# Kernel optimization log

Measured on AMD Instinct MI355X. Metric: run time of the kernel, lower is better.

The kernel has to match this reference:

```python
import jax, jax.numpy as jnp
import numpy as np
from jax import lax

B, C, H, W = 4, 24, 128, 128
R = 7
NUM_CLASSES = 6
MAX_STEPS = 8


def _conv(x, w, b, pad):
    y = lax.conv_general_dilated(x, w, (1, 1), [(pad, pad), (pad, pad)],
                                 dimension_numbers=("NCHW", "OIHW", "NCHW"))
    return y + b[None, :, None, None]


def setup_inputs() -> dict:
    key = jax.random.key(0)
    ks = jax.random.split(key, 16)
    s = 0.05
    inp = {
        "depth_latent": jax.random.normal(ks[0], (B, C, H, W), jnp.float32),
        "texture_features": jax.random.normal(ks[1], (B, 3, H, W), jnp.float32),
        "class_labels": jax.random.randint(ks[2], (B,), 0, NUM_CLASSES),
        # texture_encoder
        "w_te1": jax.random.normal(ks[3], (64, 3, 3, 3), jnp.float32) * s,
        "b_te1": jnp.zeros((64,), jnp.float32),
        "w_te2": jax.random.normal(ks[4], (128, 64, 3, 3), jnp.float32) * s,
        "b_te2": jnp.zeros((128,), jnp.float32),
        # class embedding [num_classes, 128]
        "emb": jax.random.normal(ks[5], (NUM_CLASSES, 128), jnp.float32) * s,
        # fusion_layer: Conv2d(256,256,3) -> Conv2d(256, C*R*R, 1)
        "w_f1": jax.random.normal(ks[6], (256, 256, 3, 3), jnp.float32) * s,
        "b_f1": jnp.zeros((256,), jnp.float32),
        "w_f2": jax.random.normal(ks[7], (C * R * R, 256, 1, 1), jnp.float32) * s,
        "b_f2": jnp.zeros((C * R * R,), jnp.float32),
        # class_gate: Conv2d(128,64,3) -> Conv2d(64,num_classes,1)
        "w_g1": jax.random.normal(ks[8], (64, 128, 3, 3), jnp.float32) * s,
        "b_g1": jnp.zeros((64,), jnp.float32),
        "w_g2": jax.random.normal(ks[9], (NUM_CLASSES, 64, 1, 1), jnp.float32) * s,
        "b_g2": jnp.zeros((NUM_CLASSES,), jnp.float32),
        "class_intensity": jnp.ones((1, NUM_CLASSES, 1, 1), jnp.float32),
    }
    return inp


def _forward(depth_latent, texture_features, class_labels,
             w_te1, b_te1, w_te2, b_te2, emb,
             w_f1, b_f1, w_f2, b_f2,
             w_g1, b_g1, w_g2, b_g2, class_intensity):
    pad = R // 2
    # texture encoder
    tex = jax.nn.relu(_conv(texture_features, w_te1, b_te1, 1))
    tex = jax.nn.relu(_conv(tex, w_te2, b_te2, 1))  # [B,128,H,W]

    # 1-D integer class label path
    class_cond = jax.nn.one_hot(class_labels, NUM_CLASSES, dtype=jnp.float32)[:, :, None, None]  # [B,K,1,1]
    class_emb = emb[class_labels][:, :, None, None]  # [B,128,1,1]

    gate = jax.nn.sigmoid(_conv(jax.nn.relu(_conv(tex, w_g1, b_g1, 1)), w_g2, b_g2, 0))
    class_gate = gate * class_cond  # [B,K,H,W]

    fused = jnp.concatenate([tex, jnp.broadcast_to(class_emb, (tex.shape[0], 128, H, W))], axis=1)
    weights = _conv(jax.nn.relu(_conv(fused, w_f1, b_f1, 1)), w_f2, b_f2, 0)
    weights = weights.reshape(-1, C, R * R, H, W)

    intensity_map = (class_gate * class_intensity).sum(axis=1, keepdims=True)  # [B,1,H,W]
    weights = weights * intensity_map[:, :, None]  # [B,C,R*R,H,W]
    weights = jax.nn.softmax(weights, axis=2)

    def diffusion_step(lat):
        p = jnp.pad(lat, ((0, 0), (0, 0), (pad, pad), (pad, pad)), mode="edge")
        # unfold order: kernel row-major (i*R + j)
        windows = jnp.stack([p[:, :, i:i + H, j:j + W]
                             for i in range(R) for j in range(R)], axis=2)
        return (windows * weights).sum(axis=2)

    enhanced = lax.fori_loop(0, MAX_STEPS, lambda _, lat: diffusion_step(lat), depth_latent)

    condition_map = intensity_map * class_gate.sum(axis=1, keepdims=True)
    return enhanced, class_gate, condition_map


def reference(depth_latent, texture_features, class_labels,
              w_te1, b_te1, w_te2, b_te2, emb,
              w_f1, b_f1, w_f2, b_f2,
              w_g1, b_g1, w_g2, b_g2, class_intensity):
    return _forward(depth_latent, texture_features, class_labels,
                    w_te1, b_te1, w_te2, b_te2, emb,
                    w_f1, b_f1, w_f2, b_f2,
                    w_g1, b_g1, w_g2, b_g2, class_intensity)
```

## Files before the change

kernel.cpp:

```cpp
#include <hip/hip_runtime.h>
#include <hip/hip_bf16.h>
#include <stdint.h>

#define DINL __device__ __forceinline__

DINL float bf2f(__hip_bfloat16 v) { return __bfloat162float(v); }
DINL __hip_bfloat16 f2bf(float v) { return __float2bfloat16(v); }
DINL float bflo(unsigned int u) { return __uint_as_float(u << 16); }
DINL float bfhi(unsigned int u) { return __uint_as_float(u & 0xffff0000u); }

DINL float loadf(float v) { return v; }
DINL float loadf(__hip_bfloat16 v) { return __bfloat162float(v); }

typedef __attribute__((ext_vector_type(8))) short bf16x8;
typedef __attribute__((ext_vector_type(4))) float f32x4;

#define O_WTE1 0
#define O_WG2  1792
#define O_SS   2304
#define O_INT  11520
#define BO_W2B   308224u
#define BO_TE2B 1094656u
#define BO_WG1B 1242112u
#define BO_WF1B 1389568u
#define BO_TEX  4194304u
#define BO_F1   20971520u
#define BO_PING 54525952u
#define BO_PONG 60817408u
#define BO_W    67108864u
#define BO_T1   BO_W
#define BO_G1   (BO_W + 16777216u)

__global__ __launch_bounds__(256) void prep_kernel(
    const float* __restrict__ w_te1, const float* __restrict__ w_te2,
    const float* __restrict__ w_g1,  const float* __restrict__ w_f1,
    const float* __restrict__ w_f2,  const float* __restrict__ w_g2,
    const float* __restrict__ emb,   const int* __restrict__ labels,
    float* __restrict__ wsf)
{
  const int gid = blockIdx.x * 256 + threadIdx.x;
  const int stride = gridDim.x * 256;
  const int A0 = 1728, A1 = A0 + 393216, A2 = A1 + 73728, A3 = A2 + 73728,
            A4 = A3 + 294912, A5 = A4 + 384;
  __hip_bfloat16* w2b  = (__hip_bfloat16*)((char*)wsf + BO_W2B);
  __hip_bfloat16* te2b = (__hip_bfloat16*)((char*)wsf + BO_TE2B);
  __hip_bfloat16* g1b  = (__hip_bfloat16*)((char*)wsf + BO_WG1B);
  __hip_bfloat16* f1b  = (__hip_bfloat16*)((char*)wsf + BO_WF1B);
  for (int i = gid; i < A5; i += stride) {
    if (i < A0) {
      int s = i; int o = s / 27; int r = s - o * 27; int ic = r / 9; int t = r - ic * 9;
      wsf[O_WTE1 + (((o >> 5) * 3 + ic) * 9 + t) * 32 + (o & 31)] = w_te1[s];
    } else if (i < A1) {
      int s = i - A0;
      int j = s & 7; int lane = (s >> 3) & 63; int ks = (s >> 9) & 7;
      int wv = (s >> 12) & 3; int c = s >> 14;
      int tap = wv * 16 + (lane & 15);
      int k = ks * 32 + (lane >> 4) * 8 + j;
      float v = (tap < 49) ? w_f2[(c * 49 + tap) * 256 + k] : 0.f;
      w2b[s] = f2bf(v);
    } else if (i < A2) {
      int s = i - A1;
      int k = s & 31; int n = (s >> 5) & 63; int u = s >> 11;
      int t = u % 9; int v = u / 9; int kc = v & 1; int ocg = v >> 1;
      te2b[s] = f2bf(w_te2[((ocg * 64 + n) * 64 + kc * 32 + k) * 9 + t]);
    } else if (i < A3) {
      int s = i - A2;
      int k = s & 31; int n = (s >> 5) & 63; int u = s >> 11;
      int t = u % 9; int kc = u / 9;
      g1b[s] = f2bf(w_g1[(n * 128 + kc * 32 + k) * 9 + t]);
    } else if (i < A4) {
      int s = i - A3;
      int k = s & 31; int n = (s >> 5) & 63; int u = s >> 11;
      int t = u % 9; int v = u / 9; int kc = v & 3; int ocg = v >> 2;
      f1b[s] = f2bf(w_f1[((ocg * 64 + n) * 256 + kc * 32 + k) * 9 + t]);
    } else {
      int s = i - A4;
      wsf[O_WG2 + s] = w_g2[s];
    }
  }
  if (gid < 1024) {
    int b = gid >> 8, o = gid & 255;
    int lab = labels[b];
    float St[9];
#pragma unroll
    for (int t = 0; t < 9; ++t) St[t] = 0.f;
    for (int i = 0; i < 128; ++i) {
      float e = emb[lab * 128 + i];
#pragma unroll
      for (int t = 0; t < 9; ++t)
        St[t] += w_f1[(o * 256 + 128 + i) * 9 + t] * e;
    }
#pragma unroll
    for (int ch = 0; ch < 3; ++ch)
#pragma unroll
      for (int cw = 0; cw < 3; ++cw) {
        float sum = 0.f;
#pragma unroll
        for (int t = 0; t < 9; ++t) {
          int kh = t / 3, kw = t - kh * 3;
          bool ok = !(ch == 0 && kh == 0) && !(ch == 2 && kh == 2) &&
                    !(cw == 0 && kw == 0) && !(cw == 2 && kw == 2);
          if (ok) sum += St[t];
        }
        wsf[O_SS + gid * 9 + ch * 3 + cw] = sum;
      }
  }
}

template<typename TIn, int ICH, bool PIXMAJOR>
__global__ __launch_bounds__(256, 2) void conv3x3_kernel(
    const TIn* __restrict__ in, const float* __restrict__ wf,
    const float* __restrict__ bias,
    __hip_bfloat16* __restrict__ out, const int och_total)
{
  constexpr int CH = (ICH < 16) ? ICH : 16;
  constexpr int NCHUNK = ICH / CH;
  __shared__ TIn sIn[CH][18][20];
  const int tid = threadIdx.x;
  const int b = blockIdx.z;
  const int ob = blockIdx.y;
  const int och0 = ob * 32;
  const int tileY = blockIdx.x >> 3, tileX = blockIdx.x & 7;
  const int ty = tid >> 4, tx = tid & 15;
  const int h = tileY * 16 + ty, w = tileX * 16 + tx;
  const int h0 = tileY * 16 - 1, w0 = tileX * 16 - 1;

  float acc[32];
#pragma unroll
  for (int o = 0; o < 32; ++o) acc[o] = bias[och0 + o];

  for (int cc = 0; cc < NCHUNK; ++cc) {
    if (cc) __syncthreads();
    for (int e = tid; e < CH * 324; e += 256) {
      int ic = e / 324, r = e - ic * 324;
      int y = r / 18, x = r - y * 18;
      int gh = h0 + y, gw = w0 + x;
      TIn v = TIn(0.f);
      if ((unsigned)gh < 128u && (unsigned)gw < 128u)
        v = in[((b * ICH + cc * CH + ic) << 14) + (gh << 7) + gw];
      sIn[ic][y][x] = v;
    }
    __syncthreads();
#pragma unroll 1
    for (int ic = 0; ic < CH; ++ic) {
      const float* wrow = wf + (ob * ICH + cc * CH + ic) * 288;
#pragma unroll
      for (int t = 0; t < 9; ++t) {
        const int kh = t / 3, kw = t - kh * 3;
        const float v = loadf(sIn[ic][ty + kh][tx + kw]);
#pragma unroll
        for (int o = 0; o < 32; ++o)
          acc[o] = fmaf(wrow[t * 32 + o], v, acc[o]);
      }
    }
  }

  const int pix = (h << 7) + w;
  if constexpr (!PIXMAJOR) {
#pragma unroll
    for (int o = 0; o < 32; ++o)
      out[((b * och_total + och0 + o) << 14) + pix] = f2bf(fmaxf(acc[o], 0.f));
  } else {
    union { uint4 u4[4]; __hip_bfloat16 hh[32]; } pk;
#pragma unroll
    for (int o = 0; o < 32; ++o) pk.hh[o] = f2bf(fmaxf(acc[o], 0.f));
    uint4* dst = reinterpret_cast<uint4*>(out + ((size_t)(b << 14) + pix) * och_total + och0);
#pragma unroll
    for (int i = 0; i < 4; ++i) dst[i] = pk.u4[i];
  }
}

template<int ICH, bool ADD_SS>
__global__ __launch_bounds__(256, 2) void conv3x3_mfma_kernel(
    const __hip_bfloat16* __restrict__ in, const __hip_bfloat16* __restrict__ wb,
    const float* __restrict__ bias, const float* __restrict__ SS,
    __hip_bfloat16* __restrict__ out, const int och_total)
{
  constexpr int NKC = ICH / 32;
  __shared__ __hip_bfloat16 sH[324][40];
  __shared__ __hip_bfloat16 sW[9][64][40];
  const int tid = threadIdx.x, b = blockIdx.z, ocg = blockIdx.y;
  const int tileY = blockIdx.x >> 3, tileX = blockIdx.x & 7;
  const int h0 = tileY * 16 - 1, w0 = tileX * 16 - 1;
  const int wave = tid >> 6, lane = tid & 63, m16 = lane & 15, quad = lane >> 4;

  f32x4 acc[4][4];
#pragma unroll
  for (int i = 0; i < 4; ++i)
#pragma unroll
    for (int j = 0; j < 4; ++j) acc[i][j] = f32x4{0.f, 0.f, 0.f, 0.f};

  for (int kc = 0; kc < NKC; ++kc) {
    if (kc) __syncthreads();
    for (int e = tid; e < 1296; e += 256) {
      int pos = e >> 2, q = e & 3;
      int y = pos / 18, x = pos - y * 18;
      int gh = h0 + y, gw = w0 + x;
      uint4 v = uint4{0u, 0u, 0u, 0u};
      if ((unsigned)gh < 128u && (unsigned)gw < 128u)
        v = *(const uint4*)(in + ((size_t)((b << 14) + (gh << 7) + gw)) * ICH + kc * 32 + q * 8);
      *(uint4*)&sH[pos][q * 8] = v;
    }
    const uint4* wsrc = (const uint4*)(wb + ((size_t)(ocg * NKC + kc)) * 9 * 64 * 32);
    for (int e = tid; e < 2304; e += 256) {
      int q = e & 3, n = (e >> 2) & 63, t = e >> 8;
      *(uint4*)&sW[t][n][q * 8] = wsrc[e];
    }
    __syncthreads();
#pragma unroll
    for (int t = 0; t < 9; ++t) {
      const int dy = t / 3, dx = t - dy * 3;
      bf16x8 bfr[4];
#pragma unroll
      for (int nt = 0; nt < 4; ++nt)
        bfr[nt] = *(const bf16x8*)&sW[t][nt * 16 + m16][quad * 8];
#pragma unroll
      for (int mi = 0; mi < 4; ++mi) {
        const int py = wave * 4 + mi;
        const bf16x8 afr = *(const bf16x8*)&sH[(py + dy) * 18 + dx + m16][quad * 8];
#pragma unroll
        for (int nt = 0; nt < 4; ++nt)
          acc[mi][nt] = __builtin_amdgcn_mfma_f32_16x16x32_bf16(afr, bfr[nt], acc[mi][nt], 0, 0, 0);
      }
    }
  }

  float bv[4];
#pragma unroll
  for (int nt = 0; nt < 4; ++nt) bv[nt] = bias[ocg * 64 + nt * 16 + m16];
#pragma unroll
  for (int mi = 0; mi < 4; ++mi) {
    const int py = wave * 4 + mi;
    const int h = tileY * 16 + py;
    const int chc = (h == 0) ? 0 : ((h == 127) ? 2 : 1);
#pragma unroll
    for (int nt = 0; nt < 4; ++nt) {
      float sr0 = 0.f, sr1 = 0.f, sr2 = 0.f;
      if constexpr (ADD_SS) {
        const float* sp = SS + ((size_t)(b << 8) + (ocg * 64 + nt * 16 + m16)) * 9;
        sr0 = sp[chc * 3 + 0]; sr1 = sp[chc * 3 + 1]; sr2 = sp[chc * 3 + 2];
      }
      const int och = ocg * 64 + nt * 16 + m16;
#pragma unroll
      for (int r = 0; r < 4; ++r) {
        const int px = quad * 4 + r;
        const int w = tileX * 16 + px;
        float v = acc[mi][nt][r] + bv[nt];
        if constexpr (ADD_SS)
          v += (w == 0) ? sr0 : ((w == 127) ? sr2 : sr1);
        v = fmaxf(v, 0.f);
        out[((size_t)((b << 14) + (h << 7) + w)) * och_total + och] = f2bf(v);
      }
    }
  }
}

__global__ __launch_bounds__(256) void gate2_kernel(
    const __hip_bfloat16* __restrict__ g1, const float* __restrict__ wg2,
    const float* __restrict__ b_g2, const int* __restrict__ labels,
    const float* __restrict__ ci,
    float* __restrict__ out_cg, float* __restrict__ out_cond,
    float* __restrict__ inten)
{
  const int b = blockIdx.y;
  const int pix = blockIdx.x * 256 + threadIdx.x;
  float acc[6];
#pragma unroll
  for (int k = 0; k < 6; ++k) acc[k] = b_g2[k];
  const uint4* gp = (const uint4*)(g1 + ((size_t)((b << 14) + pix)) * 64);
#pragma unroll
  for (int i4 = 0; i4 < 8; ++i4) {
    const uint4 q = gp[i4];
    const float v0 = bflo(q.x), v1 = bfhi(q.x), v2 = bflo(q.y), v3 = bfhi(q.y);
    const float v4 = bflo(q.z), v5 = bfhi(q.z), v6 = bflo(q.w), v7 = bfhi(q.w);
#pragma unroll
    for (int k = 0; k < 6; ++k) {
      const float* wr = wg2 + k * 64 + i4 * 8;
      acc[k] = fmaf(wr[0], v0, acc[k]); acc[k] = fmaf(wr[1], v1, acc[k]);
      acc[k] = fmaf(wr[2], v2, acc[k]); acc[k] = fmaf(wr[3], v3, acc[k]);
      acc[k] = fmaf(wr[4], v4, acc[k]); acc[k] = fmaf(wr[5], v5, acc[k]);
      acc[k] = fmaf(wr[6], v6, acc[k]); acc[k] = fmaf(wr[7], v7, acc[k]);
    }
  }
  const int lab = labels[b];
  float gate[6], gl = 0.f;
#pragma unroll
  for (int k = 0; k < 6; ++k) {
    gate[k] = 1.f / (1.f + __expf(-acc[k]));
    gl = (k == lab) ? gate[k] : gl;
  }
  const float civ = ci[lab];
  const float it = gl * civ;
#pragma unroll
  for (int k = 0; k < 6; ++k)
    out_cg[((b * 6 + k) << 14) + pix] = (k == lab) ? gate[k] : 0.f;
  inten[(b << 14) + pix] = it;
  out_cond[(b << 14) + pix] = it * gl;
}

__global__ __launch_bounds__(256, 2) void gemm_softmax_kernel(
    const __hip_bfloat16* __restrict__ f1, const __hip_bfloat16* __restrict__ w2b,
    const float* __restrict__ b_f2, const float* __restrict__ inten,
    __hip_bfloat16* __restrict__ wout)
{
  __shared__ float sL[49 * 65];
  __shared__ float sR1[256];
  __shared__ float sR2[256];
  const int tid = threadIdx.x;
  const int pix0 = blockIdx.x * 64;
  const int wave = tid >> 6, lane = tid & 63;
  const int m16 = lane & 15, quad = lane >> 4;

  bf16x8 afr[4][8];
#pragma unroll
  for (int mt = 0; mt < 4; ++mt)
#pragma unroll
    for (int ks = 0; ks < 8; ++ks)
      afr[mt][ks] = *(const bf16x8*)(f1 + ((size_t)(pix0 + mt * 16 + m16)) * 256 + ks * 32 + quad * 8);

  const int epix = tid & 63, tq = tid >> 6;
  const int P = pix0 + epix;
  const float s = inten[P];
  const int ob = P >> 14, op = P & 16383;

  const int ltap = wave * 16 + m16;
  const int lpixb = quad * 4;

  for (int c = 0; c < 24; ++c) {
    const bf16x8* bp = (const bf16x8*)(w2b + (((size_t)(c * 4 + wave) * 8) * 64 + lane) * 8);
    bf16x8 bfr[8];
#pragma unroll
    for (int ks = 0; ks < 8; ++ks) bfr[ks] = bp[ks * 64];

    f32x4 acc[4] = {f32x4{0,0,0,0}, f32x4{0,0,0,0}, f32x4{0,0,0,0}, f32x4{0,0,0,0}};
#pragma unroll
    for (int ks = 0; ks < 8; ++ks)
#pragma unroll
      for (int mt = 0; mt < 4; ++mt)
        acc[mt] = __builtin_amdgcn_mfma_f32_16x16x32_bf16(afr[mt][ks], bfr[ks], acc[mt], 0, 0, 0);

    const float bias_t = b_f2[c * 49 + min(ltap, 48)];
    if (ltap < 49) {
#pragma unroll
      for (int mt = 0; mt < 4; ++mt)
#pragma unroll
        for (int r = 0; r < 4; ++r)
          sL[ltap * 65 + mt * 16 + lpixb + r] = acc[mt][r] + bias_t;
    }
    __syncthreads();

    float v[13];
    float mx = -3.4e38f;
#pragma unroll
    for (int i = 0; i < 13; ++i) {
      const int t = tq * 13 + i;
      if (t < 49) { v[i] = sL[t * 65 + epix] * s; mx = fmaxf(mx, v[i]); }
    }
    sR1[tq * 64 + epix] = mx;
    __syncthreads();
    mx = fmaxf(fmaxf(sR1[epix], sR1[64 + epix]), fmaxf(sR1[128 + epix], sR1[192 + epix]));

    float sum = 0.f;
#pragma unroll
    for (int i = 0; i < 13; ++i) {
      const int t = tq * 13 + i;
      if (t < 49) { v[i] = __expf(v[i] - mx); sum += v[i]; }
    }
    sR2[tq * 64 + epix] = sum;
    __syncthreads();
    const float tot = sR2[epix] + sR2[64 + epix] + sR2[128 + epix] + sR2[192 + epix];
    const float rs = 1.f / tot;

    __hip_bfloat16* wo = wout + (((size_t)(ob * 24 + c) * 49) << 14) + op;
#pragma unroll
    for (int i = 0; i < 13; ++i) {
      const int t = tq * 13 + i;
      if (t < 49) wo[(size_t)t << 14] = f2bf(v[i] * rs);
    }
  }
}

__global__ __launch_bounds__(256) void diff_kernel(
    const float* __restrict__ lin, const __hip_bfloat16* __restrict__ wts,
    float* __restrict__ lout)
{
  __shared__ float sT[10][70];
  const int bc = blockIdx.z;
  const int w0 = blockIdx.x * 64, h0 = blockIdx.y * 4;
  const int tid = threadIdx.y * 64 + threadIdx.x;
  for (int e = tid; e < 700; e += 256) {
    int y = e / 70, x = e - y * 70;
    int gh = min(max(h0 - 3 + y, 0), 127), gw = min(max(w0 - 3 + x, 0), 127);
    sT[y][x] = lin[(bc << 14) + (gh << 7) + gw];
  }
  __syncthreads();
  const int tx = threadIdx.x, ty = threadIdx.y;
  const int pix = ((h0 + ty) << 7) + w0 + tx;
  const __hip_bfloat16* wp = wts + (((size_t)bc * 49) << 14) + pix;
  float acc = 0.f;
#pragma unroll
  for (int t = 0; t < 49; ++t) {
    const int kh = t / 7, kw = t - kh * 7;
    acc = fmaf(bf2f(wp[(size_t)t << 14]), sT[ty + kh][tx + kw], acc);
  }
  lout[(bc << 14) + pix] = acc;
}

extern "C" void kernel_launch(void* const* d_in, const int* in_sizes, int n_in,
                              void* d_out, int out_size, void* d_ws, size_t ws_size,
                              hipStream_t stream)
{
  const float* depth = (const float*)d_in[0];
  const float* texf  = (const float*)d_in[1];
  const int*   labels= (const int*)d_in[2];
  const float* w_te1 = (const float*)d_in[3];
  const float* b_te1 = (const float*)d_in[4];
  const float* w_te2 = (const float*)d_in[5];
  const float* b_te2 = (const float*)d_in[6];
  const float* emb   = (const float*)d_in[7];
  const float* w_f1  = (const float*)d_in[8];
  const float* b_f1  = (const float*)d_in[9];
  const float* w_f2  = (const float*)d_in[10];
  const float* b_f2  = (const float*)d_in[11];
  const float* w_g1  = (const float*)d_in[12];
  const float* b_g1  = (const float*)d_in[13];
  const float* w_g2  = (const float*)d_in[14];
  const float* b_g2  = (const float*)d_in[15];
  const float* ci    = (const float*)d_in[16];

  char*  ws  = (char*)d_ws;
  float* wsf = (float*)d_ws;
  __hip_bfloat16* w2bf  = (__hip_bfloat16*)(ws + BO_W2B);
  __hip_bfloat16* te2bf = (__hip_bfloat16*)(ws + BO_TE2B);
  __hip_bfloat16* g1bf  = (__hip_bfloat16*)(ws + BO_WG1B);
  __hip_bfloat16* f1bf  = (__hip_bfloat16*)(ws + BO_WF1B);
  __hip_bfloat16* tex   = (__hip_bfloat16*)(ws + BO_TEX);
  __hip_bfloat16* f1    = (__hip_bfloat16*)(ws + BO_F1);
  float* ping           = (float*)(ws + BO_PING);
  float* pong           = (float*)(ws + BO_PONG);
  __hip_bfloat16* wts   = (__hip_bfloat16*)(ws + BO_W);
  __hip_bfloat16* t1    = (__hip_bfloat16*)(ws + BO_T1);
  __hip_bfloat16* g1    = (__hip_bfloat16*)(ws + BO_G1);

  float* out      = (float*)d_out;
  float* out_enh  = out;
  float* out_cg   = out + 1572864;
  float* out_cond = out + 1966080;

  prep_kernel<<<512, 256, 0, stream>>>(w_te1, w_te2, w_g1, w_f1, w_f2, w_g2, emb, labels, wsf);
  conv3x3_kernel<float, 3, true><<<dim3(64, 2, 4), 256, 0, stream>>>(texf, wsf + O_WTE1, b_te1, t1, 64);
  conv3x3_mfma_kernel<64,  false><<<dim3(64, 2, 4), 256, 0, stream>>>(t1,  te2bf, b_te2, nullptr,      tex, 128);
  conv3x3_mfma_kernel<128, false><<<dim3(64, 1, 4), 256, 0, stream>>>(tex, g1bf,  b_g1,  nullptr,      g1,  64);
  gate2_kernel<<<dim3(64, 4), 256, 0, stream>>>(g1, wsf + O_WG2, b_g2, labels, ci, out_cg, out_cond, wsf + O_INT);
  conv3x3_mfma_kernel<128, true ><<<dim3(64, 4, 4), 256, 0, stream>>>(tex, f1bf,  b_f1,  wsf + O_SS,   f1,  256);
  gemm_softmax_kernel<<<dim3(1024), 256, 0, stream>>>(f1, w2bf, b_f2, wsf + O_INT, wts);

  dim3 dgrid(2, 32, 96), dblk(64, 4, 1);
  diff_kernel<<<dgrid, dblk, 0, stream>>>(depth, wts, ping);
  diff_kernel<<<dgrid, dblk, 0, stream>>>(ping, wts, pong);
  diff_kernel<<<dgrid, dblk, 0, stream>>>(pong, wts, ping);
  diff_kernel<<<dgrid, dblk, 0, stream>>>(ping, wts, pong);
  diff_kernel<<<dgrid, dblk, 0, stream>>>(pong, wts, ping);
  diff_kernel<<<dgrid, dblk, 0, stream>>>(ping, wts, pong);
  diff_kernel<<<dgrid, dblk, 0, stream>>>(pong, wts, ping);
  diff_kernel<<<dgrid, dblk, 0, stream>>>(ping, wts, out_enh);
}
```

Before: 608.7 us.

## Transpose GEMM so taps are rows, softmax via lane shuffles, split channels across grid

Swaps the MFMA operand roles so the weight tile supplies the 16-tap rows and each wave owns 16 pixels. The whole 49-tap softmax for a pixel then sits inside one wave and reduces with two xor shuffles, which removes the shared-memory staging and three block barriers per channel. Channels are split across a second grid dimension (6 groups of 4), and the launch bound is raised to 4 blocks per CU for occupancy. The cost is that each block reloads its pixel fragments and the weight fragments are read straight from global memory inside the loop.

```diff
diff --git a/kernel.cpp b/kernel.cpp
--- a/kernel.cpp
+++ b/kernel.cpp
@@ -53,8 +53,8 @@
     } else if (i < A1) {
       int s = i - A0;
       int j = s & 7; int lane = (s >> 3) & 63; int ks = (s >> 9) & 7;
-      int wv = (s >> 12) & 3; int c = s >> 14;
-      int tap = wv * 16 + (lane & 15);
+      int mt = (s >> 12) & 3; int c = s >> 14;
+      int tap = mt * 16 + (lane & 15);
       int k = ks * 32 + (lane >> 4) * 8 + j;
       float v = (tap < 49) ? w_f2[(c * 49 + tap) * 256 + k] : 0.f;
       w2b[s] = f2bf(v);
@@ -298,85 +298,74 @@
   out_cond[(b << 14) + pix] = it * gl;
 }
 
-__global__ __launch_bounds__(256, 2) void gemm_softmax_kernel(
+__global__ __launch_bounds__(256, 4) void gemm_softmax_kernel(
     const __hip_bfloat16* __restrict__ f1, const __hip_bfloat16* __restrict__ w2b,
     const float* __restrict__ b_f2, const float* __restrict__ inten,
     __hip_bfloat16* __restrict__ wout)
 {
-  __shared__ float sL[49 * 65];
-  __shared__ float sR1[256];
-  __shared__ float sR2[256];
   const int tid = threadIdx.x;
   const int pix0 = blockIdx.x * 64;
+  const int c0 = blockIdx.y * 4;
   const int wave = tid >> 6, lane = tid & 63;
-  const int m16 = lane & 15, quad = lane >> 4;
-
-  bf16x8 afr[4][8];
-#pragma unroll
-  for (int mt = 0; mt < 4; ++mt)
-#pragma unroll
-    for (int ks = 0; ks < 8; ++ks)
-      afr[mt][ks] = *(const bf16x8*)(f1 + ((size_t)(pix0 + mt * 16 + m16)) * 256 + ks * 32 + quad * 8);
-
-  const int epix = tid & 63, tq = tid >> 6;
-  const int P = pix0 + epix;
-  const float s = inten[P];
-  const int ob = P >> 14, op = P & 16383;
-
-  const int ltap = wave * 16 + m16;
-  const int lpixb = quad * 4;
-
-  for (int c = 0; c < 24; ++c) {
-    const bf16x8* bp = (const bf16x8*)(w2b + (((size_t)(c * 4 + wave) * 8) * 64 + lane) * 8);
-    bf16x8 bfr[8];
-#pragma unroll
-    for (int ks = 0; ks < 8; ++ks) bfr[ks] = bp[ks * 64];
-
-    f32x4 acc[4] = {f32x4{0,0,0,0}, f32x4{0,0,0,0}, f32x4{0,0,0,0}, f32x4{0,0,0,0}};
-#pragma unroll
-    for (int ks = 0; ks < 8; ++ks)
-#pragma unroll
-      for (int mt = 0; mt < 4; ++mt)
-        acc[mt] = __builtin_amdgcn_mfma_f32_16x16x32_bf16(afr[mt][ks], bfr[ks], acc[mt], 0, 0, 0);
-
-    const float bias_t = b_f2[c * 49 + min(ltap, 48)];
-    if (ltap < 49) {
-#pragma unroll
-      for (int mt = 0; mt < 4; ++mt)
-#pragma unroll
-        for (int r = 0; r < 4; ++r)
-          sL[ltap * 65 + mt * 16 + lpixb + r] = acc[mt][r] + bias_t;
-    }
-    __syncthreads();
-
-    float v[13];
+  const int n16 = lane & 15, quad = lane >> 4;
+  const int p = pix0 + wave * 16 + n16;
+
+  bf16x8 bfr[8];
+#pragma unroll
+  for (int ks = 0; ks < 8; ++ks)
+    bfr[ks] = *(const bf16x8*)(f1 + (size_t)p * 256 + ks * 32 + quad * 8);
+
+  const float s = inten[p];
+  const int ob = p >> 14, op = p & 16383;
+
+#pragma unroll 1
+  for (int cl = 0; cl < 4; ++cl) {
+    const int c = c0 + cl;
+    f32x4 acc[4];
+#pragma unroll
+    for (int mt = 0; mt < 4; ++mt) {
+      acc[mt] = f32x4{0.f, 0.f, 0.f, 0.f};
+      const bf16x8* amt = (const bf16x8*)w2b + (((size_t)(c * 4 + mt)) * 8) * 64 + lane;
+#pragma unroll
+      for (int ks = 0; ks < 8; ++ks)
+        acc[mt] = __builtin_amdgcn_mfma_f32_16x16x32_bf16(amt[ks * 64], bfr[ks], acc[mt], 0, 0, 0);
+    }
+
+    float v[4][4];
     float mx = -3.4e38f;
 #pragma unroll
-    for (int i = 0; i < 13; ++i) {
-      const int t = tq * 13 + i;
-      if (t < 49) { v[i] = sL[t * 65 + epix] * s; mx = fmaxf(mx, v[i]); }
-    }
-    sR1[tq * 64 + epix] = mx;
-    __syncthreads();
-    mx = fmaxf(fmaxf(sR1[epix], sR1[64 + epix]), fmaxf(sR1[128 + epix], sR1[192 + epix]));
-
+    for (int mt = 0; mt < 4; ++mt)
+#pragma unroll
+      for (int r = 0; r < 4; ++r) {
+        const int tap = mt * 16 + quad * 4 + r;
+        const bool ok = tap < 49;
+        const float lv = ok ? (acc[mt][r] + b_f2[c * 49 + (ok ? tap : 0)]) * s : -3.4e38f;
+        v[mt][r] = lv;
+        mx = fmaxf(mx, lv);
+      }
+    mx = fmaxf(mx, __shfl_xor(mx, 16, 64));
+    mx = fmaxf(mx, __shfl_xor(mx, 32, 64));
     float sum = 0.f;
 #pragma unroll
-    for (int i = 0; i < 13; ++i) {
-      const int t = tq * 13 + i;
-      if (t < 49) { v[i] = __expf(v[i] - mx); sum += v[i]; }
-    }
-    sR2[tq * 64 + epix] = sum;
-    __syncthreads();
-    const float tot = sR2[epix] + sR2[64 + epix] + sR2[128 + epix] + sR2[192 + epix];
-    const float rs = 1.f / tot;
+    for (int mt = 0; mt < 4; ++mt)
+#pragma unroll
+      for (int r = 0; r < 4; ++r) {
+        const float e = __expf(v[mt][r] - mx);
+        v[mt][r] = e;
+        sum += e;
+      }
+    sum += __shfl_xor(sum, 16, 64);
+    sum += __shfl_xor(sum, 32, 64);
+    const float rs = 1.f / sum;
 
     __hip_bfloat16* wo = wout + (((size_t)(ob * 24 + c) * 49) << 14) + op;
 #pragma unroll
-    for (int i = 0; i < 13; ++i) {
-      const int t = tq * 13 + i;
-      if (t < 49) wo[(size_t)t << 14] = f2bf(v[i] * rs);
-    }
+    for (int mt = 0; mt < 4; ++mt)
+#pragma unroll
+      for (int r = 0; r < 4; ++r) {
+        const int tap = mt * 16 + quad * 4 + r;
+        if (tap < 49) wo[(size_t)tap << 14] = f2bf(v[mt][r] * rs);
+      }
   }
 }
 
@@ -453,7 +442,7 @@
   conv3x3_mfma_kernel<128, false><<<dim3(64, 1, 4), 256, 0, stream>>>(tex, g1bf,  b_g1,  nullptr,      g1,  64);
   gate2_kernel<<<dim3(64, 4), 256, 0, stream>>>(g1, wsf + O_WG2, b_g2, labels, ci, out_cg, out_cond, wsf + O_INT);
   conv3x3_mfma_kernel<128, true ><<<dim3(64, 4, 4), 256, 0, stream>>>(tex, f1bf,  b_f1,  wsf + O_SS,   f1,  256);
-  gemm_softmax_kernel<<<dim3(1024), 256, 0, stream>>>(f1, w2bf, b_f2, wsf + O_INT, wts);
+  gemm_softmax_kernel<<<dim3(1024, 6), 256, 0, stream>>>(f1, w2bf, b_f2, wsf + O_INT, wts);
 
   dim3 dgrid(2, 32, 96), dblk(64, 4, 1);
   diff_kernel<<<dgrid, dblk, 0, stream>>>(depth, wts, ping);
```

New measurement: 630.1 us. 3.5% more time.
